# Kernel optimization log

Measured on AMD Instinct MI355X. Metric: run time of the kernel, lower is better.

The kernel has to match this reference:

```python
import jax, jax.numpy as jnp
import numpy as np

S, T, B, E, H, V = 64, 64, 64, 256, 256, 32000
PAD = 0


def _lstm_layer(X, Wih, Whh, b, h0, c0):
    # X: (time, B, in), torch gate order i,f,g,o
    def step(carry, x_t):
        h, c = carry
        z = x_t @ Wih.T + h @ Whh.T + b
        i, f, g, o = jnp.split(z, 4, axis=-1)
        c = jax.nn.sigmoid(f) * c + jax.nn.sigmoid(i) * jnp.tanh(g)
        h = jax.nn.sigmoid(o) * jnp.tanh(c)
        return (h, c), h
    (hT, cT), outs = jax.lax.scan(step, (h0, c0), X)
    return outs, hT, cT


def setup_inputs() -> dict:
    key = jax.random.key(0)
    ks = jax.random.split(key, 20)
    p = lambda k, shape: (jax.random.normal(k, shape, jnp.float32) * 0.05)
    inp = {
        "source_padded": jax.random.randint(ks[0], (S, B), 0, V, jnp.int32),
        "target_padded": jax.random.randint(ks[1], (T, B), 0, V, jnp.int32),
        "src_emb": p(ks[2], (V, E)),
        "tgt_emb": p(ks[3], (V, E)),
        "enc_Wih_f": p(ks[4], (4 * H, E)),
        "enc_Whh_f": p(ks[5], (4 * H, H)),
        "enc_b_f": p(ks[6], (4 * H,)),
        "enc_Wih_b": p(ks[7], (4 * H, E)),
        "enc_Whh_b": p(ks[8], (4 * H, H)),
        "enc_b_b": p(ks[9], (4 * H,)),
        "dec_Wih": p(ks[10], (4 * H, E + H)),
        "dec_Whh": p(ks[11], (4 * H, H)),
        "dec_b": p(ks[12], (4 * H,)),
        "Wh": p(ks[13], (H, 2 * H)),
        "Wc": p(ks[14], (H, 2 * H)),
        "Watt": p(ks[15], (H, 2 * H)),
        "Wcomb": p(ks[16], (H, 3 * H)),
        "Wvocab": p(ks[17], (V, H)),
    }
    return inp


def reference(source_padded, target_padded, src_emb, tgt_emb,
              enc_Wih_f, enc_Whh_f, enc_b_f, enc_Wih_b, enc_Whh_b, enc_b_b,
              dec_Wih, dec_Whh, dec_b, Wh, Wc, Watt, Wcomb, Wvocab):
    X = src_emb[source_padded]                      # (S,B,E)
    h0 = jnp.zeros((B, H), X.dtype)
    c0 = jnp.zeros((B, H), X.dtype)
    # bidirectional encoder (all sequences full length -> pack is identity)
    fwd_out, hf, cf = _lstm_layer(X, enc_Wih_f, enc_Whh_f, enc_b_f, h0, c0)
    bwd_out, hb, cb = _lstm_layer(X[::-1], enc_Wih_b, enc_Whh_b, enc_b_b, h0, c0)
    bwd_out = bwd_out[::-1]
    enc_hiddens = jnp.concatenate([fwd_out, bwd_out], -1).transpose(1, 0, 2)  # (B,S,2H)
    dec_h = jnp.concatenate([hf, hb], -1) @ Wh.T     # h_projection
    dec_c = jnp.concatenate([cf, cb], -1) @ Wc.T     # c_projection
    enc_proj = enc_hiddens @ Watt.T                  # (B,S,H)

    Y = tgt_emb[target_padded[:-1]]                  # (T-1,B,E)

    def dstep(carry, Y_t):
        h, c, o_prev = carry
        x = jnp.concatenate([Y_t, o_prev], -1)       # (B,E+H)
        z = x @ dec_Wih.T + h @ dec_Whh.T + dec_b
        i, f, g, o = jnp.split(z, 4, axis=-1)
        c = jax.nn.sigmoid(f) * c + jax.nn.sigmoid(i) * jnp.tanh(g)
        h = jax.nn.sigmoid(o) * jnp.tanh(c)
        e_t = jnp.einsum('bsh,bh->bs', enc_proj, h)  # attention scores
        alpha = jax.nn.softmax(e_t, axis=-1)         # no pads -> mask is no-op
        a_t = jnp.einsum('bs,bsd->bd', alpha, enc_hiddens)  # context (B,2H)
        O_t = jnp.tanh(jnp.concatenate([a_t, h], -1) @ Wcomb.T)  # dropout=eval
        return (h, c, O_t), O_t

    _, outs = jax.lax.scan(dstep, (dec_h, dec_c, jnp.zeros((B, H), X.dtype)), Y)
    P = jax.nn.log_softmax(outs @ Wvocab.T, axis=-1)          # (T-1,B,V)
    gold = jnp.take_along_axis(P, target_padded[1:][..., None], axis=-1)[..., 0]
    tmask = (target_padded[1:] != PAD).astype(P.dtype)
    return (gold * tmask).sum(axis=0)                          # (B,)
```

## Files before the change

### kernel.cpp

```cpp
#include <hip/hip_runtime.h>
#include <hip/hip_bf16.h>

static constexpr int S = 64, T = 64, B = 64, E = 256, H = 256, V = 32000;
static constexpr int H4 = 4 * H;
static constexpr int NCHUNK = 500;
static constexpr int NROW = (T - 1) * B;
static constexpr int LDP = 264;

typedef short bf16x8 __attribute__((ext_vector_type(8)));
typedef float f32x4 __attribute__((ext_vector_type(4)));
typedef unsigned long long ull;

__device__ __forceinline__ float sigf(float x) { return 1.0f / (1.0f + __expf(-x)); }
__device__ __forceinline__ float tanhfast(float x) { return 1.0f - 2.0f / (__expf(2.0f * x) + 1.0f); }
__device__ __forceinline__ float bflo(uint w) { return __uint_as_float(w << 16); }
__device__ __forceinline__ float bfhi(uint w) { return __uint_as_float(w & 0xffff0000u); }
__device__ __forceinline__ ushort f2bu(float x) {
  return __bfloat16_as_ushort(__float2bfloat16(x));
}

__device__ __forceinline__ void st_u32(uint* p, uint v) {
  __hip_atomic_store(p, v, __ATOMIC_RELAXED, __HIP_MEMORY_SCOPE_AGENT);
}
__device__ __forceinline__ uint ld_u32(const uint* p) {
  return __hip_atomic_load(p, __ATOMIC_RELAXED, __HIP_MEMORY_SCOPE_AGENT);
}

__global__ __launch_bounds__(256) void k_cvt_bf16(const float* __restrict__ src,
                                                  __hip_bfloat16* __restrict__ dst, int n) {
  int i = blockIdx.x * 256 + threadIdx.x;
  if (i < n) dst[i] = __float2bfloat16(src[i]);
}

__global__ __launch_bounds__(256) void k_cvt_slice(const float* __restrict__ src,
                                                   __hip_bfloat16* __restrict__ dst) {
  int n = blockIdx.x, tid = threadIdx.x;
  dst[n * 256 + tid] = __float2bfloat16(src[n * 512 + tid]);
}

__global__ __launch_bounds__(256) void k_gather(const int* __restrict__ idx,
                                                const float* __restrict__ emb,
                                                __hip_bfloat16* __restrict__ dst) {
  int r = blockIdx.x, tid = threadIdx.x;
  dst[r * 256 + tid] = __float2bfloat16(emb[idx[r] * E + tid]);
}

__global__ __launch_bounds__(256) void k_pack4(const float* __restrict__ src,
                                               uint2* __restrict__ dst,
                                               int total, int jshift, int ld, int off) {
  int idx = blockIdx.x * 256 + threadIdx.x;
  if (idx >= total) return;
  int J = 1 << jshift;
  int i = idx >> jshift, j = idx & (J - 1);
  const float* s = src + (size_t)j * ld + off + 4 * i;
  float4 v = *(const float4*)s;
  uint2 o;
  o.x = (uint)f2bu(v.x) | ((uint)f2bu(v.y) << 16);
  o.y = (uint)f2bu(v.z) | ((uint)f2bu(v.w) << 16);
  dst[(size_t)i * J + j] = o;
}

#define MFMA_TILE_BODY(Abase, Wbase, rb, cb)                                     \
  const int tid = threadIdx.x;                                                   \
  const int lane = tid & 63, wid = tid >> 6;                                     \
  const int wr = wid >> 1, wc = wid & 1;                                         \
  const int l15 = lane & 15, l4 = lane >> 4;                                     \
  for (int it = 0; it < 8; it++) {                                               \
    int c = it * 256 + tid;                                                      \
    int row = c >> 5, off = (c & 31) * 8;                                        \
    *(uint4*)&Asl[row * LDP + off] =                                             \
        *(const uint4*)((Abase) + (size_t)((rb) + row) * 256 + off);             \
    *(uint4*)&Bsl[row * LDP + off] =                                             \
        *(const uint4*)((Wbase) + (size_t)((cb) + row) * 256 + off);             \
  }                                                                              \
  __syncthreads();                                                               \
  f32x4 acc[2][2];                                                               \
  for (int m = 0; m < 2; m++)                                                    \
    for (int n = 0; n < 2; n++) acc[m][n] = (f32x4){0.f, 0.f, 0.f, 0.f};         \
  for (int kk = 0; kk < 8; kk++) {                                               \
    int ko = kk * 32 + l4 * 8;                                                   \
    bf16x8 a0 = *(const bf16x8*)&Asl[(wr * 32 + l15) * LDP + ko];                \
    bf16x8 a1 = *(const bf16x8*)&Asl[(wr * 32 + 16 + l15) * LDP + ko];           \
    bf16x8 b0 = *(const bf16x8*)&Bsl[(wc * 32 + l15) * LDP + ko];                \
    bf16x8 b1 = *(const bf16x8*)&Bsl[(wc * 32 + 16 + l15) * LDP + ko];           \
    acc[0][0] = __builtin_amdgcn_mfma_f32_16x16x32_bf16(a0, b0, acc[0][0], 0, 0, 0); \
    acc[0][1] = __builtin_amdgcn_mfma_f32_16x16x32_bf16(a0, b1, acc[0][1], 0, 0, 0); \
    acc[1][0] = __builtin_amdgcn_mfma_f32_16x16x32_bf16(a1, b0, acc[1][0], 0, 0, 0); \
    acc[1][1] = __builtin_amdgcn_mfma_f32_16x16x32_bf16(a1, b1, acc[1][1], 0, 0, 0); \
  }

__global__ __launch_bounds__(256) void k_gemm_bias(
    const __hip_bfloat16* __restrict__ A, const __hip_bfloat16* __restrict__ W,
    const float* __restrict__ bias, float* __restrict__ C, int ldc) {
  __shared__ __align__(16) ushort Asl[64 * LDP];
  __shared__ __align__(16) ushort Bsl[64 * LDP];
  const int cb = blockIdx.x * 64, rb = blockIdx.y * 64;
  MFMA_TILE_BODY((const ushort*)A, (const ushort*)W, rb, cb)
  #pragma unroll
  for (int m = 0; m < 2; m++)
    #pragma unroll
    for (int n = 0; n < 2; n++) {
      int col = cb + wc * 32 + n * 16 + l15;
      float bv = bias[col];
      #pragma unroll
      for (int r = 0; r < 4; r++) {
        int row = rb + wr * 32 + m * 16 + l4 * 4 + r;
        C[(size_t)row * ldc + col] = acc[m][n][r] + bv;
      }
    }
}

__global__ __launch_bounds__(256) void k_encproj_mfma(
    const __hip_bfloat16* __restrict__ fwd_bf, const __hip_bfloat16* __restrict__ bwd_bf,
    const __hip_bfloat16* __restrict__ Watt_bf, __hip_bfloat16* __restrict__ encproj_bf) {
  __shared__ __align__(16) ushort Asl[64 * LDP];
  __shared__ __align__(16) ushort Bsl[64 * LDP];
  const int cb = blockIdx.x * 64, rb = blockIdx.y * 64;
  const int tid = threadIdx.x;
  const int lane = tid & 63, wid = tid >> 6;
  const int wr = wid >> 1, wc = wid & 1;
  const int l15 = lane & 15, l4 = lane >> 4;
  f32x4 acc[2][2];
  #pragma unroll
  for (int m = 0; m < 2; m++)
    #pragma unroll
    for (int n = 0; n < 2; n++) acc[m][n] = (f32x4){0.f, 0.f, 0.f, 0.f};
  for (int kt = 0; kt < 2; kt++) {
    if (kt) __syncthreads();
    for (int it = 0; it < 8; it++) {
      int c = it * 256 + tid;
      int row = c >> 5, off = (c & 31) * 8;
      int r = rb + row, s = r >> 6, bb = r & 63;
      const ushort* arow = (kt == 0)
          ? (const ushort*)fwd_bf + (size_t)(s * 64 + bb) * 256
          : (const ushort*)bwd_bf + (size_t)(s * 64 + bb) * 256;
      *(uint4*)&Asl[row * LDP + off] = *(const uint4*)(arow + off);
      *(uint4*)&Bsl[row * LDP + off] =
          *(const uint4*)((const ushort*)Watt_bf + (size_t)(cb + row) * 512 + kt * 256 + off);
    }
    __syncthreads();
    for (int kk = 0; kk < 8; kk++) {
      int ko = kk * 32 + l4 * 8;
      bf16x8 a0 = *(const bf16x8*)&Asl[(wr * 32 + l15) * LDP + ko];
      bf16x8 a1 = *(const bf16x8*)&Asl[(wr * 32 + 16 + l15) * LDP + ko];
      bf16x8 b0 = *(const bf16x8*)&Bsl[(wc * 32 + l15) * LDP + ko];
      bf16x8 b1 = *(const bf16x8*)&Bsl[(wc * 32 + 16 + l15) * LDP + ko];
      acc[0][0] = __builtin_amdgcn_mfma_f32_16x16x32_bf16(a0, b0, acc[0][0], 0, 0, 0);
      acc[0][1] = __builtin_amdgcn_mfma_f32_16x16x32_bf16(a0, b1, acc[0][1], 0, 0, 0);
      acc[1][0] = __builtin_amdgcn_mfma_f32_16x16x32_bf16(a1, b0, acc[1][0], 0, 0, 0);
      acc[1][1] = __builtin_amdgcn_mfma_f32_16x16x32_bf16(a1, b1, acc[1][1], 0, 0, 0);
    }
  }
  #pragma unroll
  for (int m = 0; m < 2; m++)
    #pragma unroll
    for (int n = 0; n < 2; n++) {
      int col = cb + wc * 32 + n * 16 + l15;
      #pragma unroll
      for (int r = 0; r < 4; r++) {
        int row = rb + wr * 32 + m * 16 + l4 * 4 + r;
        int s = row >> 6, bb = row & 63;
        ((ushort*)encproj_bf)[(size_t)(bb * 64 + s) * 256 + col] = f2bu(acc[m][n][r]);
      }
    }
}

__global__ __launch_bounds__(256) void k_vocab2(
    const __hip_bfloat16* __restrict__ outs_bf, const __hip_bfloat16* __restrict__ Wv,
    const int* __restrict__ tgt, float* __restrict__ part_max,
    float* __restrict__ part_sum, float* __restrict__ gold) {
  __shared__ __align__(16) ushort Asl[64 * LDP];
  __shared__ __align__(16) ushort Bsl[64 * LDP];
  __shared__ int goldcol[64];
  __shared__ float pm[64][2], ps[64][2];
  const int vb = blockIdx.x;
  const int tid = threadIdx.x;
  const int lane = tid & 63, wid = tid >> 6;
  const int wr = wid >> 1, wc = wid & 1;
  const int l15 = lane & 15, l4 = lane >> 4;
  for (int it = 0; it < 8; it++) {
    int c = it * 256 + tid;
    int row = c >> 5, off = (c & 31) * 8;
    *(uint4*)&Bsl[row * LDP + off] =
        *(const uint4*)((const ushort*)Wv + (size_t)(vb * 64 + row) * 256 + off);
  }
  for (int t = 0; t < T - 1; t++) {
    __syncthreads();
    for (int it = 0; it < 8; it++) {
      int c = it * 256 + tid;
      int row = c >> 5, off = (c & 31) * 8;
      *(uint4*)&Asl[row * LDP + off] =
          *(const uint4*)((const ushort*)outs_bf + (size_t)(t * 64 + row) * 256 + off);
    }
    if (tid < 64) goldcol[tid] = tgt[(t + 1) * B + tid];
    __syncthreads();
    f32x4 acc[2][2];
    #pragma unroll
    for (int m = 0; m < 2; m++)
      #pragma unroll
      for (int n = 0; n < 2; n++) acc[m][n] = (f32x4){0.f, 0.f, 0.f, 0.f};
    for (int kk = 0; kk < 8; kk++) {
      int ko = kk * 32 + l4 * 8;
      bf16x8 a0 = *(const bf16x8*)&Asl[(wr * 32 + l15) * LDP + ko];
      bf16x8 a1 = *(const bf16x8*)&Asl[(wr * 32 + 16 + l15) * LDP + ko];
      bf16x8 b0 = *(const bf16x8*)&Bsl[(wc * 32 + l15) * LDP + ko];
      bf16x8 b1 = *(const bf16x8*)&Bsl[(wc * 32 + 16 + l15) * LDP + ko];
      acc[0][0] = __builtin_amdgcn_mfma_f32_16x16x32_bf16(a0, b0, acc[0][0], 0, 0, 0);
      acc[0][1] = __builtin_amdgcn_mfma_f32_16x16x32_bf16(a0, b1, acc[0][1], 0, 0, 0);
      acc[1][0] = __builtin_amdgcn_mfma_f32_16x16x32_bf16(a1, b0, acc[1][0], 0, 0, 0);
      acc[1][1] = __builtin_amdgcn_mfma_f32_16x16x32_bf16(a1, b1, acc[1][1], 0, 0, 0);
    }
    #pragma unroll
    for (int m = 0; m < 2; m++) {
      #pragma unroll
      for (int r = 0; r < 4; r++) {
        int row_local = wr * 32 + m * 16 + l4 * 4 + r;
        int gc = goldcol[row_local];
        #pragma unroll
        for (int n = 0; n < 2; n++) {
          int col = vb * 64 + wc * 32 + n * 16 + l15;
          if (col == gc) gold[t * 64 + row_local] = acc[m][n][r];
        }
        float v = fmaxf(acc[m][0][r], acc[m][1][r]);
        #pragma unroll
        for (int o = 1; o < 16; o <<= 1) v = fmaxf(v, __shfl_xor(v, o));
        float e = __expf(acc[m][0][r] - v) + __expf(acc[m][1][r] - v);
        #pragma unroll
        for (int o = 1; o < 16; o <<= 1) e += __shfl_xor(e, o);
        if (l15 == 0) { pm[row_local][wc] = v; ps[row_local][wc] = e; }
      }
    }
    __syncthreads();
    if (tid < 64) {
      float m0 = pm[tid][0], m1 = pm[tid][1];
      float M = fmaxf(m0, m1);
      float Ss = ps[tid][0] * __expf(m0 - M) + ps[tid][1] * __expf(m1 - M);
      part_max[(size_t)vb * NROW + t * 64 + tid] = M;
      part_sum[(size_t)vb * NROW + t * 64 + tid] = Ss;
    }
  }
}

__global__ __launch_bounds__(256) void k_enc4(
    const float* __restrict__ XwF, const float* __restrict__ XwB,
    const float* __restrict__ WhhF, const float* __restrict__ WhhB,
    uint* __restrict__ Xenc_u32,
    __hip_bfloat16* __restrict__ fwd_bf, __hip_bfloat16* __restrict__ bwd_bf,
    float* __restrict__ Cfin, uint* __restrict__ eflags) {
  __shared__ __align__(16) ushort Wl[128 * 264];
  __shared__ __align__(16) ushort Xa[16 * 264];
  __shared__ float zz[4][8][33];
  __shared__ float hsb[8][32];
  const int id = blockIdx.x;
  const int g = id & 7, kb = id >> 3;
  const int dir = kb >> 3, s = kb & 7;
  const int tid = threadIdx.x;
  const float* Whh = dir ? WhhB : WhhF;
  const float* Xw = dir ? XwB : XwF;
  uint* fl = eflags + (size_t)(g * 2 + dir) * 8 * 32;
  for (int i = tid; i < 128 * 256; i += 256) {
    int c = i >> 8, k2 = i & 255;
    int gate = c >> 5, jj = c & 31;
    Wl[c * 264 + k2] = f2bu(Whh[(size_t)(gate * 256 + s * 32 + jj) * 256 + k2]);
  }
  for (int i = tid; i < 16 * 264; i += 256) Xa[i] = 0;
  const int lane = tid & 63, w = tid >> 6;
  const int l15 = lane & 15, l4 = lane >> 4;
  const int tb = tid >> 5, tjj = tid & 31;
  float c_reg = 0.f;
  __syncthreads();
  for (int st = 0; st < 64; st++) {
    const int ts = dir ? 63 - st : st;
    const int par = st & 1;
    const uint* Xr = Xenc_u32 + (size_t)(par * 2 + dir) * 8192;
    uint* Xo = Xenc_u32 + (size_t)((par ^ 1) * 2 + dir) * 8192;
    for (int i = tid; i < 8 * 128; i += 256) {
      int row = i >> 7, colu = i & 127;
      uint v = ld_u32(Xr + (size_t)(8 * g + row) * 128 + colu);
      *(uint*)&Xa[row * 264 + colu * 2] = v;
    }
    __syncthreads();
    f32x4 a0v = (f32x4){0.f, 0.f, 0.f, 0.f}, a1v = (f32x4){0.f, 0.f, 0.f, 0.f};
    for (int kk = 0; kk < 8; kk++) {
      bf16x8 af = *(const bf16x8*)&Xa[l15 * 264 + kk * 32 + l4 * 8];
      bf16x8 b0 = *(const bf16x8*)&Wl[((2 * w) * 16 + l15) * 264 + kk * 32 + l4 * 8];
      bf16x8 b1 = *(const bf16x8*)&Wl[((2 * w + 1) * 16 + l15) * 264 + kk * 32 + l4 * 8];
      a0v = __builtin_amdgcn_mfma_f32_16x16x32_bf16(af, b0, a0v, 0, 0, 0);
      a1v = __builtin_amdgcn_mfma_f32_16x16x32_bf16(af, b1, a1v, 0, 0, 0);
    }
    if (l4 < 2) {
      #pragma unroll
      for (int r = 0; r < 4; r++) {
        int b = l4 * 4 + r;
        zz[w][b][l15] = a0v[r];
        zz[w][b][16 + l15] = a1v[r];
      }
    }
    __syncthreads();
    {
      int gb = 8 * g + tb, j = 32 * s + tjj;
      const float* xw = Xw + (size_t)(ts * 64 + gb) * 1024;
      float zi = zz[0][tb][tjj] + xw[j];
      float zf = zz[1][tb][tjj] + xw[256 + j];
      float zg = zz[2][tb][tjj] + xw[512 + j];
      float zo = zz[3][tb][tjj] + xw[768 + j];
      float c = sigf(zf) * c_reg + sigf(zi) * tanhfast(zg);
      c_reg = c;
      float h = sigf(zo) * tanhfast(c);
      hsb[tb][tjj] = h;
      ushort hb = f2bu(h);
      if (dir == 0) ((ushort*)fwd_bf)[(size_t)(st * 64 + gb) * 256 + j] = hb;
      else          ((ushort*)bwd_bf)[(size_t)((63 - st) * 64 + gb) * 256 + j] = hb;
    }
    __syncthreads();
    if (tid < 128) {
      int tb2 = tid >> 4, p = tid & 15;
      uint v = (uint)f2bu(hsb[tb2][2 * p]) | ((uint)f2bu(hsb[tb2][2 * p + 1]) << 16);
      st_u32(Xo + (size_t)(8 * g + tb2) * 128 + 16 * s + p, v);
    }
    __syncthreads();
    if (tid == 0) st_u32(&fl[s * 32], (uint)(st + 1));
    if (tid < 8)
      while (ld_u32(&fl[tid * 32]) < (uint)(st + 1)) __builtin_amdgcn_s_sleep(2);
    asm volatile("" ::: "memory");
    __syncthreads();
  }
  Cfin[(size_t)(dir * 64 + 8 * g + tb) * 256 + 32 * s + tjj] = c_reg;
}

__global__ __launch_bounds__(256) void k_dec_init3(
    const __hip_bfloat16* __restrict__ Xenc, const float* __restrict__ Cfin,
    const float* __restrict__ Wh, const float* __restrict__ Wc,
    uint* __restrict__ Xd_u32, float* __restrict__ decc0) {
  int b = blockIdx.x, tid = threadIdx.x;
  __shared__ __align__(16) float ch[512], cc[512];
  __shared__ float hh[256];
  ch[tid]       = __bfloat162float(Xenc[(size_t)(0 * 64 + b) * 256 + tid]);
  ch[256 + tid] = __bfloat162float(Xenc[(size_t)(1 * 64 + b) * 256 + tid]);
  cc[tid]       = Cfin[(size_t)(0 * 64 + b) * 256 + tid];
  cc[256 + tid] = Cfin[(size_t)(1 * 64 + b) * 256 + tid];
  __syncthreads();
  const float* wh = Wh + tid * 512;
  const float* wc = Wc + tid * 512;
  float ah = 0, ac = 0;
  for (int k = 0; k < 512; k += 4) {
    float4 hv = *(const float4*)&ch[k];
    float4 cv = *(const float4*)&cc[k];
    float4 w1 = *(const float4*)&wh[k];
    float4 w2 = *(const float4*)&wc[k];
    ah += hv.x * w1.x + hv.y * w1.y + hv.z * w1.z + hv.w * w1.w;
    ac += cv.x * w2.x + cv.y * w2.y + cv.z * w2.z + cv.w * w2.w;
  }
  decc0[b * 256 + tid] = ac;
  hh[tid] = ah;
  __syncthreads();
  if (tid < 128) {
    uint v = (uint)f2bu(hh[2 * tid]) | ((uint)f2bu(hh[2 * tid + 1]) << 16);
    Xd_u32[(size_t)b * 256 + tid] = v;
    Xd_u32[(size_t)b * 256 + 128 + tid] = 0u;
  }
}

__global__ __launch_bounds__(512) void k_dec6(
    const float* __restrict__ YW, const float* __restrict__ dWih,
    const float* __restrict__ dWhh, const uint2* __restrict__ Wcq,
    const __hip_bfloat16* __restrict__ encproj_bf,
    const __hip_bfloat16* __restrict__ fwd_bf, const __hip_bfloat16* __restrict__ bwd_bf,
    const float* __restrict__ decc0, uint* __restrict__ Xd_u32,
    __hip_bfloat16* __restrict__ outs_bf,
    uint* __restrict__ zflags, uint* __restrict__ aflags) {
  __shared__ __align__(16) char smem[155648];
  const int id = blockIdx.x;
  const int g = id & 7, kb = id >> 3;
  const int tid = threadIdx.x;
  uint* zfl = zflags + (size_t)g * 8 * 32;
  uint* afl = aflags + (size_t)g * 16 * 32;

  if (kb < 8) {
    const int s = kb;
    ushort* Wl = (ushort*)smem;
    ushort* Xa = (ushort*)(smem + 133120);
    float* zslds = (float*)(smem + 149760);
    float* hsb = (float*)(smem + 153856);
    for (int i = tid; i < 128 * 512; i += 512) {
      int c = i >> 9, k2 = i & 511;
      int gate = c >> 5, jj = c & 31;
      int gr = gate * 256 + 32 * s + jj;
      float v = (k2 < 256) ? dWhh[(size_t)gr * 256 + k2]
                           : dWih[(size_t)gr * 512 + 256 + (k2 - 256)];
      Wl[c * 520 + k2] = f2bu(v);
    }
    for (int i = tid; i < 16 * 520; i += 512) Xa[i] = 0;
    const int lane = tid & 63, w = tid >> 6;
    const int l15 = lane & 15, l4 = lane >> 4;
    float c_reg = 0.f;
    if (tid < 256) {
      int b = tid >> 5, jj = tid & 31;
      c_reg = decc0[(size_t)(8 * g + b) * 256 + 32 * s + jj];
    }
    __syncthreads();
    for (int i = tid; i < 8 * 128; i += 512) {
      int row = i >> 7, p = i & 127;
      uint v = ld_u32(Xd_u32 + (size_t)(8 * g + row) * 256 + p);
      *(uint*)&Xa[row * 520 + 2 * p] = v;
    }
    __syncthreads();
    f32x4 accv = (f32x4){0.f, 0.f, 0.f, 0.f};
    for (int kk = 0; kk < 8; kk++) {
      bf16x8 af = *(const bf16x8*)&Xa[l15 * 520 + kk * 32 + l4 * 8];
      bf16x8 bf = *(const bf16x8*)&Wl[(w * 16 + l15) * 520 + kk * 32 + l4 * 8];
      accv = __builtin_amdgcn_mfma_f32_16x16x32_bf16(af, bf, accv, 0, 0, 0);
    }
    for (int t = 0; t < 63; t++) {
      const int par = t & 1;
      if (t > 0) {
        if (tid < 16)
          while (ld_u32(&afl[tid * 32]) < (uint)t) __builtin_amdgcn_s_sleep(1);
        asm volatile("" ::: "memory");
        __syncthreads();
      }
      for (int i = tid; i < 8 * 128; i += 512) {
        int row = i >> 7, p = i & 127;
        uint v = ld_u32(Xd_u32 + (size_t)par * 16384 + (size_t)(8 * g + row) * 256 + 128 + p);
        *(uint*)&Xa[row * 520 + 256 + 2 * p] = v;
      }
      __syncthreads();
      for (int kk = 8; kk < 16; kk++) {
        bf16x8 af = *(const bf16x8*)&Xa[l15 * 520 + kk * 32 + l4 * 8];
        bf16x8 bf = *(const bf16x8*)&Wl[(w * 16 + l15) * 520 + kk * 32 + l4 * 8];
        accv = __builtin_amdgcn_mfma_f32_16x16x32_bf16(af, bf, accv, 0, 0, 0);
      }
      if (l4 < 2) {
        #pragma unroll
        for (int r = 0; r < 4; r++) {
          int b = l4 * 4 + r;
          zslds[b * 128 + w * 16 + l15] = accv[r];
        }
      }
      __syncthreads();
      if (tid < 256) {
        int b = tid >> 5, jj = tid & 31;
        int gb = 8 * g + b;
        const float* yw = YW + (size_t)(t * 64 + gb) * 1024 + 32 * s + jj;
        float zi = zslds[b * 128 + jj] + yw[0];
        float zf = zslds[b * 128 + 32 + jj] + yw[256];
        float zg = zslds[b * 128 + 64 + jj] + yw[512];
        float zo = zslds[b * 128 + 96 + jj] + yw[768];
        float c = sigf(zf) * c_reg + sigf(zi) * tanhfast(zg);
        c_reg = c;
        hsb[b * 32 + jj] = sigf(zo) * tanhfast(c);
      }
      __syncthreads();
      if (tid < 128) {
        int b = tid >> 4, p = tid & 15;
        uint v = (uint)f2bu(hsb[b * 32 + 2 * p]) | ((uint)f2bu(hsb[b * 32 + 2 * p + 1]) << 16);
        st_u32(Xd_u32 + (size_t)(par ^ 1) * 16384 + (size_t)(8 * g + b) * 256 + 16 * s + p, v);
      }
      __syncthreads();
      if (tid == 0) st_u32(&zfl[s * 32], (uint)(t + 1));
      if (t < 62) {
        if (tid < 8)
          while (ld_u32(&zfl[tid * 32]) < (uint)(t + 1)) __builtin_amdgcn_s_sleep(1);
        asm volatile("" ::: "memory");
        __syncthreads();
        for (int i = tid; i < 8 * 128; i += 512) {
          int row = i >> 7, p = i & 127;
          uint v = ld_u32(Xd_u32 + (size_t)(par ^ 1) * 16384 + (size_t)(8 * g + row) * 256 + p);
          *(uint*)&Xa[row * 520 + 2 * p] = v;
        }
        __syncthreads();
        accv = (f32x4){0.f, 0.f, 0.f, 0.f};
        for (int kk = 0; kk < 8; kk++) {
          bf16x8 af = *(const bf16x8*)&Xa[l15 * 520 + kk * 32 + l4 * 8];
          bf16x8 bf = *(const bf16x8*)&Wl[(w * 16 + l15) * 520 + kk * 32 + l4 * 8];
          accv = __builtin_amdgcn_mfma_f32_16x16x32_bf16(af, bf, accv, 0, 0, 0);
        }
      }
    }
  } else {
    const int lb = (kb - 8) >> 1, jh = (kb - 8) & 1;
    const int b = 8 * g + lb;
    ushort* ep = (ushort*)smem;
    ushort* eh = (ushort*)(smem + 33792);
    float* hn = (float*)(smem + 100352);
    float* xcomb = (float*)(smem + 101376);
    float* e_l = (float*)(smem + 104448);
    float* alpha_l = (float*)(smem + 104704);
    float* op_l = (float*)(smem + 104960);
    float* Ost = (float*)(smem + 107008);
    for (int i = tid; i < 64 * 256; i += 512) {
      int s2 = i >> 8, k2 = i & 255;
      ep[s2 * 264 + k2] = ((const ushort*)encproj_bf)[(size_t)(b * 64 + s2) * 256 + k2];
    }
    for (int i = tid; i < 64 * 512; i += 512) {
      int s2 = i >> 9, d = i & 511;
      ushort v = (d < 256) ? ((const ushort*)fwd_bf)[(size_t)(s2 * 64 + b) * 256 + d]
                           : ((const ushort*)bwd_bf)[(size_t)(s2 * 64 + b) * 256 + d - 256];
      eh[s2 * 520 + d] = v;
    }
    __syncthreads();
    for (int t = 0; t < 63; t++) {
      if (tid < 8)
        while (ld_u32(&zfl[tid * 32]) < (uint)(t + 1)) __builtin_amdgcn_s_sleep(1);
      asm volatile("" ::: "memory");
      __syncthreads();
      if (tid < 128) {
        uint v = ld_u32(Xd_u32 + (size_t)((t & 1) ^ 1) * 16384 + (size_t)b * 256 + tid);
        hn[2 * tid] = bflo(v);
        hn[2 * tid + 1] = bfhi(v);
      }
      __syncthreads();
      {
        int s2 = tid >> 3, q8 = tid & 7;
        const ushort* pr = ep + s2 * 264 + q8 * 32;
        const float* hq = hn + q8 * 32;
        float a = 0.f;
        #pragma unroll 8
        for (int kk = 0; kk < 32; kk += 2) {
          uint wv = *(const uint*)(pr + kk);
          a += bflo(wv) * hq[kk] + bfhi(wv) * hq[kk + 1];
        }
        a += __shfl_xor(a, 1);
        a += __shfl_xor(a, 2);
        a += __shfl_xor(a, 4);
        if (q8 == 0) e_l[s2] = a;
      }
      __syncthreads();
      if (tid < 64) {
        float e = e_l[tid];
        float mx = e;
        #pragma unroll
        for (int o = 32; o > 0; o >>= 1) mx = fmaxf(mx, __shfl_xor(mx, o));
        float p = __expf(e - mx);
        float ss = p;
        #pragma unroll
        for (int o = 32; o > 0; o >>= 1) ss += __shfl_xor(ss, o);
        alpha_l[tid] = p / ss;
      }
      __syncthreads();
      {
        float a = 0.f;
        const ushort* col = eh + tid;
        #pragma unroll 8
        for (int s2 = 0; s2 < 64; s2++)
          a += alpha_l[s2] * __uint_as_float(((uint)col[s2 * 520]) << 16);
        xcomb[tid] = a;
        if (tid < 256) xcomb[512 + tid] = hn[tid];
      }
      __syncthreads();
      {
        int jl = tid & 127, kq = tid >> 7;
        int j = jh * 128 + jl;
        const uint2* wp = Wcq + (size_t)(kq * 48) * 256 + j;
        const float4* x4 = (const float4*)xcomb + kq * 48;
        float a = 0.f;
        #pragma unroll 6
        for (int ii = 0; ii < 48; ii++) {
          uint2 wv = wp[(size_t)ii * 256];
          float4 xv = x4[ii];
          a += bflo(wv.x) * xv.x + bfhi(wv.x) * xv.y + bflo(wv.y) * xv.z + bfhi(wv.y) * xv.w;
        }
        op_l[kq * 128 + jl] = a;
      }
      __syncthreads();
      if (tid < 128) {
        float sum = op_l[tid] + op_l[128 + tid] + op_l[256 + tid] + op_l[384 + tid];
        float O = tanhfast(sum);
        Ost[tid] = O;
        ((ushort*)outs_bf)[(size_t)(t * 64 + b) * 256 + jh * 128 + tid] = f2bu(O);
      }
      __syncthreads();
      if (tid < 64) {
        uint v = (uint)f2bu(Ost[2 * tid]) | ((uint)f2bu(Ost[2 * tid + 1]) << 16);
        st_u32(Xd_u32 + (size_t)((t & 1) ^ 1) * 16384 + (size_t)b * 256 + 128 + jh * 64 + tid, v);
      }
      __syncthreads();
      if (tid == 0) st_u32(&afl[(lb * 2 + jh) * 32], (uint)(t + 1));
    }
  }
}

__global__ __launch_bounds__(256) void k_final(
    const float* __restrict__ part_max, const float* __restrict__ part_sum,
    const float* __restrict__ gold, const int* __restrict__ tgt,
    float* __restrict__ out) {
  int b = blockIdx.x, tid = threadIdx.x;
  int tq = tid >> 2, q = tid & 3;
  __shared__ float lm[64][4], ls[64][4];
  __shared__ float red[64];
  if (tq < T - 1) {
    int n = tq * B + b;
    float m = -__builtin_inff(), s = 0;
    for (int i = q; i < NCHUNK; i += 4) {
      float pmv = part_max[(size_t)i * NROW + n];
      float psv = part_sum[(size_t)i * NROW + n];
      float M2 = fmaxf(m, pmv);
      s = s * __expf(m - M2) + psv * __expf(pmv - M2);
      m = M2;
    }
    lm[tq][q] = m;
    ls[tq][q] = s;
  }
  __syncthreads();
  if (tid < T - 1) {
    float M = fmaxf(fmaxf(lm[tid][0], lm[tid][1]), fmaxf(lm[tid][2], lm[tid][3]));
    float Ss = ls[tid][0] * __expf(lm[tid][0] - M) + ls[tid][1] * __expf(lm[tid][1] - M) +
               ls[tid][2] * __expf(lm[tid][2] - M) + ls[tid][3] * __expf(lm[tid][3] - M);
    float lse = M + logf(Ss);
    int g = tgt[(tid + 1) * B + b];
    red[tid] = (g != 0) ? (gold[tid * B + b] - lse) : 0.f;
  }
  if (tid == T - 1) red[T - 1] = 0.f;
  __syncthreads();
  if (tid == 0) {
    float s = 0;
    for (int i = 0; i < T - 1; i++) s += red[i];
    out[b] = s;
  }
}

extern "C" void kernel_launch(void* const* d_in, const int* in_sizes, int n_in,
                              void* d_out, int out_size, void* d_ws, size_t ws_size,
                              hipStream_t stream) {
  (void)in_sizes; (void)n_in; (void)out_size; (void)ws_size;
  const int*   src   = (const int*)  d_in[0];
  const int*   tgt   = (const int*)  d_in[1];
  const float* semb  = (const float*)d_in[2];
  const float* temb  = (const float*)d_in[3];
  const float* WihF  = (const float*)d_in[4];
  const float* WhhF  = (const float*)d_in[5];
  const float* bF    = (const float*)d_in[6];
  const float* WihB  = (const float*)d_in[7];
  const float* WhhB  = (const float*)d_in[8];
  const float* bB    = (const float*)d_in[9];
  const float* dWih  = (const float*)d_in[10];
  const float* dWhh  = (const float*)d_in[11];
  const float* db    = (const float*)d_in[12];
  const float* Wh    = (const float*)d_in[13];
  const float* Wc    = (const float*)d_in[14];
  const float* Watt  = (const float*)d_in[15];
  const float* Wcomb = (const float*)d_in[16];
  const float* Wv    = (const float*)d_in[17];
  float* out = (float*)d_out;

  char* wp = (char*)d_ws;
  auto alloc = [&](size_t bytes) -> char* {
    char* p = wp;
    wp += (bytes + 255) & ~(size_t)255;
    return p;
  };
  float* XwF  = (float*)alloc((size_t)S * B * H4 * 4);
  float* XwB  = (float*)alloc((size_t)S * B * H4 * 4);
  float* YW   = (float*)alloc((size_t)(T - 1) * B * H4 * 4);
  __hip_bfloat16* fwd_bf     = (__hip_bfloat16*)alloc((size_t)S * B * H * 2);
  __hip_bfloat16* bwd_bf     = (__hip_bfloat16*)alloc((size_t)S * B * H * 2);
  __hip_bfloat16* encproj_bf = (__hip_bfloat16*)alloc((size_t)B * S * H * 2);
  __hip_bfloat16* Ag         = (__hip_bfloat16*)alloc((size_t)S * B * E * 2);
  __hip_bfloat16* Yg         = (__hip_bfloat16*)alloc((size_t)(T - 1) * B * E * 2);
  __hip_bfloat16* WihF_bf    = (__hip_bfloat16*)alloc((size_t)H4 * E * 2);
  __hip_bfloat16* WihB_bf    = (__hip_bfloat16*)alloc((size_t)H4 * E * 2);
  __hip_bfloat16* dWih_bf    = (__hip_bfloat16*)alloc((size_t)H4 * E * 2);
  __hip_bfloat16* Wv_bf      = (__hip_bfloat16*)alloc((size_t)V * H * 2);
  __hip_bfloat16* Watt_bf    = (__hip_bfloat16*)alloc((size_t)H * 512 * 2);
  __hip_bfloat16* outs_bf    = (__hip_bfloat16*)alloc((size_t)NROW * H * 2);
  uint2* Wcq = (uint2*)alloc((size_t)192 * 256 * 8);
  float* part_max = (float*)alloc((size_t)NCHUNK * NROW * 4);
  float* part_sum = (float*)alloc((size_t)NCHUNK * NROW * 4);
  float* gold     = (float*)alloc((size_t)NROW * 4);
  float* Cfin  = (float*)alloc((size_t)2 * B * H * 4);
  float* decc0 = (float*)alloc((size_t)B * H * 4);
  __hip_bfloat16* Xenc = (__hip_bfloat16*)alloc((size_t)2 * 2 * B * H * 2);
  uint* Xdec = (uint*)alloc((size_t)2 * B * 256 * 4);
  char* stateBase = wp;
  uint* eflags = (uint*)alloc(16 * 8 * 32 * 4);
  uint* zflags = (uint*)alloc(8 * 8 * 32 * 4);
  uint* aflags = (uint*)alloc(8 * 16 * 32 * 4);
  size_t stateBytes = (size_t)(wp - stateBase);
  hipMemsetAsync(stateBase, 0, stateBytes, stream);
  hipMemsetAsync(Xenc, 0, (size_t)2 * 2 * B * H * 2, stream);

  hipLaunchKernelGGL(k_cvt_bf16, dim3((H4 * E + 255) / 256), dim3(256), 0, stream,
                     WihF, WihF_bf, H4 * E);
  hipLaunchKernelGGL(k_cvt_bf16, dim3((H4 * E + 255) / 256), dim3(256), 0, stream,
                     WihB, WihB_bf, H4 * E);
  hipLaunchKernelGGL(k_cvt_slice, dim3(H4), dim3(256), 0, stream, dWih, dWih_bf);
  hipLaunchKernelGGL(k_cvt_bf16, dim3((V * H + 255) / 256), dim3(256), 0, stream,
                     Wv, Wv_bf, V * H);
  hipLaunchKernelGGL(k_cvt_bf16, dim3((H * 512 + 255) / 256), dim3(256), 0, stream,
                     Watt, Watt_bf, H * 512);
  hipLaunchKernelGGL(k_gather, dim3(S * B), dim3(256), 0, stream, src, semb, Ag);
  hipLaunchKernelGGL(k_gather, dim3((T - 1) * B), dim3(256), 0, stream, tgt, temb, Yg);
  hipLaunchKernelGGL(k_pack4, dim3(192 * 256 / 256), dim3(256), 0, stream,
                     Wcomb, Wcq, 192 * 256, 8, 768, 0);

  hipLaunchKernelGGL(k_gemm_bias, dim3(H4 / 64, S * B / 64), dim3(256), 0, stream,
                     Ag, WihF_bf, bF, XwF, H4);
  hipLaunchKernelGGL(k_gemm_bias, dim3(H4 / 64, S * B / 64), dim3(256), 0, stream,
                     Ag, WihB_bf, bB, XwB, H4);
  hipLaunchKernelGGL(k_gemm_bias, dim3(H4 / 64, (T - 1) * B / 64), dim3(256), 0, stream,
                     Yg, dWih_bf, db, YW, H4);

  hipLaunchKernelGGL(k_enc4, dim3(128), dim3(256), 0, stream,
                     XwF, XwB, WhhF, WhhB, (uint*)Xenc, fwd_bf, bwd_bf, Cfin, eflags);
  hipLaunchKernelGGL(k_dec_init3, dim3(B), dim3(256), 0, stream,
                     Xenc, Cfin, Wh, Wc, Xdec, decc0);
  hipLaunchKernelGGL(k_encproj_mfma, dim3(4, 64), dim3(256), 0, stream,
                     fwd_bf, bwd_bf, Watt_bf, encproj_bf);

  hipLaunchKernelGGL(k_dec6, dim3(192), dim3(512), 0, stream,
                     YW, dWih, dWhh, Wcq, encproj_bf, fwd_bf, bwd_bf,
                     decc0, Xdec, outs_bf, zflags, aflags);

  hipLaunchKernelGGL(k_vocab2, dim3(NCHUNK), dim3(256), 0, stream,
                     outs_bf, Wv_bf, tgt, part_max, part_sum, gold);
  hipLaunchKernelGGL(k_final, dim3(B), dim3(256), 0, stream,
                     part_max, part_sum, gold, tgt, out);
}
```

Baseline: 1.209 ms.

## Fuse embedding gather and weight conversion into GEMMs and encoder kernel

The embedding gather and the fp32-to-bf16 weight casts now happen inside the input-projection GEMM's shared-memory load, so the separate conversion and gather kernels and their intermediate buffers go away. The Wv, Watt and Wcomb conversions run on 64 extra blocks added to the encoder recurrence kernel, overlapping with the serial LSTM work. The decoder input projection is launched after the encoder. In the encoder and decoder steps, hidden-state bf16 packing now pairs values with a lane shuffle and stores them directly, removing an LDS staging buffer and one barrier per step. The extra blocks compete with the encoder recurrence for resources, and the GEMMs now re-read fp32 weights once per tile.

```diff
diff --git a/kernel.cpp b/kernel.cpp
--- a/kernel.cpp
+++ b/kernel.cpp
@@ -18,6 +18,9 @@
 __device__ __forceinline__ ushort f2bu(float x) {
   return __bfloat16_as_ushort(__float2bfloat16(x));
 }
+__device__ __forceinline__ uint packbf(float a, float b) {
+  return (uint)f2bu(a) | ((uint)f2bu(b) << 16);
+}
 
 __device__ __forceinline__ void st_u32(uint* p, uint v) {
   __hip_atomic_store(p, v, __ATOMIC_RELAXED, __HIP_MEMORY_SCOPE_AGENT);
@@ -26,76 +29,52 @@
   return __hip_atomic_load(p, __ATOMIC_RELAXED, __HIP_MEMORY_SCOPE_AGENT);
 }
 
-__global__ __launch_bounds__(256) void k_cvt_bf16(const float* __restrict__ src,
-                                                  __hip_bfloat16* __restrict__ dst, int n) {
-  int i = blockIdx.x * 256 + threadIdx.x;
-  if (i < n) dst[i] = __float2bfloat16(src[i]);
-}
-
-__global__ __launch_bounds__(256) void k_cvt_slice(const float* __restrict__ src,
-                                                   __hip_bfloat16* __restrict__ dst) {
-  int n = blockIdx.x, tid = threadIdx.x;
-  dst[n * 256 + tid] = __float2bfloat16(src[n * 512 + tid]);
-}
-
-__global__ __launch_bounds__(256) void k_gather(const int* __restrict__ idx,
-                                                const float* __restrict__ emb,
-                                                __hip_bfloat16* __restrict__ dst) {
-  int r = blockIdx.x, tid = threadIdx.x;
-  dst[r * 256 + tid] = __float2bfloat16(emb[idx[r] * E + tid]);
-}
-
-__global__ __launch_bounds__(256) void k_pack4(const float* __restrict__ src,
-                                               uint2* __restrict__ dst,
-                                               int total, int jshift, int ld, int off) {
-  int idx = blockIdx.x * 256 + threadIdx.x;
-  if (idx >= total) return;
-  int J = 1 << jshift;
-  int i = idx >> jshift, j = idx & (J - 1);
-  const float* s = src + (size_t)j * ld + off + 4 * i;
-  float4 v = *(const float4*)s;
-  uint2 o;
-  o.x = (uint)f2bu(v.x) | ((uint)f2bu(v.y) << 16);
-  o.y = (uint)f2bu(v.z) | ((uint)f2bu(v.w) << 16);
-  dst[(size_t)i * J + j] = o;
-}
-
-#define MFMA_TILE_BODY(Abase, Wbase, rb, cb)                                     \
-  const int tid = threadIdx.x;                                                   \
-  const int lane = tid & 63, wid = tid >> 6;                                     \
-  const int wr = wid >> 1, wc = wid & 1;                                         \
-  const int l15 = lane & 15, l4 = lane >> 4;                                     \
-  for (int it = 0; it < 8; it++) {                                               \
-    int c = it * 256 + tid;                                                      \
-    int row = c >> 5, off = (c & 31) * 8;                                        \
-    *(uint4*)&Asl[row * LDP + off] =                                             \
-        *(const uint4*)((Abase) + (size_t)((rb) + row) * 256 + off);             \
-    *(uint4*)&Bsl[row * LDP + off] =                                             \
-        *(const uint4*)((Wbase) + (size_t)((cb) + row) * 256 + off);             \
-  }                                                                              \
-  __syncthreads();                                                               \
-  f32x4 acc[2][2];                                                               \
-  for (int m = 0; m < 2; m++)                                                    \
-    for (int n = 0; n < 2; n++) acc[m][n] = (f32x4){0.f, 0.f, 0.f, 0.f};         \
-  for (int kk = 0; kk < 8; kk++) {                                               \
-    int ko = kk * 32 + l4 * 8;                                                   \
-    bf16x8 a0 = *(const bf16x8*)&Asl[(wr * 32 + l15) * LDP + ko];                \
-    bf16x8 a1 = *(const bf16x8*)&Asl[(wr * 32 + 16 + l15) * LDP + ko];           \
-    bf16x8 b0 = *(const bf16x8*)&Bsl[(wc * 32 + l15) * LDP + ko];                \
-    bf16x8 b1 = *(const bf16x8*)&Bsl[(wc * 32 + 16 + l15) * LDP + ko];           \
-    acc[0][0] = __builtin_amdgcn_mfma_f32_16x16x32_bf16(a0, b0, acc[0][0], 0, 0, 0); \
-    acc[0][1] = __builtin_amdgcn_mfma_f32_16x16x32_bf16(a0, b1, acc[0][1], 0, 0, 0); \
-    acc[1][0] = __builtin_amdgcn_mfma_f32_16x16x32_bf16(a1, b0, acc[1][0], 0, 0, 0); \
-    acc[1][1] = __builtin_amdgcn_mfma_f32_16x16x32_bf16(a1, b1, acc[1][1], 0, 0, 0); \
-  }
-
-__global__ __launch_bounds__(256) void k_gemm_bias(
-    const __hip_bfloat16* __restrict__ A, const __hip_bfloat16* __restrict__ W,
-    const float* __restrict__ bias, float* __restrict__ C, int ldc) {
+__global__ __launch_bounds__(256) void k_gemm_gather(
+    const int* __restrict__ idx, const float* __restrict__ emb,
+    const float* __restrict__ W, int wld, const float* __restrict__ bias,
+    float* __restrict__ C, int ldc) {
   __shared__ __align__(16) ushort Asl[64 * LDP];
   __shared__ __align__(16) ushort Bsl[64 * LDP];
   const int cb = blockIdx.x * 64, rb = blockIdx.y * 64;
-  MFMA_TILE_BODY((const ushort*)A, (const ushort*)W, rb, cb)
+  const int tid = threadIdx.x;
+  const int lane = tid & 63, wid = tid >> 6;
+  const int wr = wid >> 1, wc = wid & 1;
+  const int l15 = lane & 15, l4 = lane >> 4;
+  for (int it = 0; it < 8; it++) {
+    int c = it * 256 + tid;
+    int row = c >> 5, off = (c & 31) * 8;
+    const float* asrc = emb + (size_t)idx[rb + row] * 256 + off;
+    float4 a0 = *(const float4*)asrc;
+    float4 a1 = *(const float4*)(asrc + 4);
+    uint4 av;
+    av.x = packbf(a0.x, a0.y); av.y = packbf(a0.z, a0.w);
+    av.z = packbf(a1.x, a1.y); av.w = packbf(a1.z, a1.w);
+    *(uint4*)&Asl[row * LDP + off] = av;
+    const float* bsrc = W + (size_t)(cb + row) * wld + off;
+    float4 b0 = *(const float4*)bsrc;
+    float4 b1 = *(const float4*)(bsrc + 4);
+    uint4 bv;
+    bv.x = packbf(b0.x, b0.y); bv.y = packbf(b0.z, b0.w);
+    bv.z = packbf(b1.x, b1.y); bv.w = packbf(b1.z, b1.w);
+    *(uint4*)&Bsl[row * LDP + off] = bv;
+  }
+  __syncthreads();
+  f32x4 acc[2][2];
+  #pragma unroll
+  for (int m = 0; m < 2; m++)
+    #pragma unroll
+    for (int n = 0; n < 2; n++) acc[m][n] = (f32x4){0.f, 0.f, 0.f, 0.f};
+  for (int kk = 0; kk < 8; kk++) {
+    int ko = kk * 32 + l4 * 8;
+    bf16x8 a0 = *(const bf16x8*)&Asl[(wr * 32 + l15) * LDP + ko];
+    bf16x8 a1 = *(const bf16x8*)&Asl[(wr * 32 + 16 + l15) * LDP + ko];
+    bf16x8 b0 = *(const bf16x8*)&Bsl[(wc * 32 + l15) * LDP + ko];
+    bf16x8 b1 = *(const bf16x8*)&Bsl[(wc * 32 + 16 + l15) * LDP + ko];
+    acc[0][0] = __builtin_amdgcn_mfma_f32_16x16x32_bf16(a0, b0, acc[0][0], 0, 0, 0);
+    acc[0][1] = __builtin_amdgcn_mfma_f32_16x16x32_bf16(a0, b1, acc[0][1], 0, 0, 0);
+    acc[1][0] = __builtin_amdgcn_mfma_f32_16x16x32_bf16(a1, b0, acc[1][0], 0, 0, 0);
+    acc[1][1] = __builtin_amdgcn_mfma_f32_16x16x32_bf16(a1, b1, acc[1][1], 0, 0, 0);
+  }
   #pragma unroll
   for (int m = 0; m < 2; m++)
     #pragma unroll
@@ -166,7 +145,7 @@
 }
 
 __global__ __launch_bounds__(256) void k_vocab2(
-    const __hip_bfloat16* __restrict__ outs_bf, const __hip_bfloat16* __restrict__ Wv,
+    const uint* __restrict__ outs_u, const __hip_bfloat16* __restrict__ Wv,
     const int* __restrict__ tgt, float* __restrict__ part_max,
     float* __restrict__ part_sum, float* __restrict__ gold) {
   __shared__ __align__(16) ushort Asl[64 * LDP];
@@ -186,11 +165,10 @@
   }
   for (int t = 0; t < T - 1; t++) {
     __syncthreads();
-    for (int it = 0; it < 8; it++) {
-      int c = it * 256 + tid;
-      int row = c >> 5, off = (c & 31) * 8;
-      *(uint4*)&Asl[row * LDP + off] =
-          *(const uint4*)((const ushort*)outs_bf + (size_t)(t * 64 + row) * 256 + off);
+    for (int i = tid; i < 64 * 128; i += 256) {
+      int row = i >> 7, colu = i & 127;
+      uint v = outs_u[(size_t)(t * 64 + row) * 128 + colu];
+      *(uint*)&Asl[row * LDP + colu * 2] = v;
     }
     if (tid < 64) goldcol[tid] = tgt[(t + 1) * B + tid];
     __syncthreads();
@@ -241,20 +219,43 @@
   }
 }
 
-__global__ __launch_bounds__(256) void k_enc4(
+__global__ __launch_bounds__(256) void k_enc4w(
     const float* __restrict__ XwF, const float* __restrict__ XwB,
     const float* __restrict__ WhhF, const float* __restrict__ WhhB,
     uint* __restrict__ Xenc_u32,
     __hip_bfloat16* __restrict__ fwd_bf, __hip_bfloat16* __restrict__ bwd_bf,
-    float* __restrict__ Cfin, uint* __restrict__ eflags) {
+    float* __restrict__ Cfin, uint* __restrict__ eflags,
+    const float* __restrict__ Wv, __hip_bfloat16* __restrict__ Wv_bf,
+    const float* __restrict__ Watt, __hip_bfloat16* __restrict__ Watt_bf,
+    const float* __restrict__ Wcomb, uint2* __restrict__ Wcq) {
   __shared__ __align__(16) ushort Wl[128 * 264];
   __shared__ __align__(16) ushort Xa[16 * 264];
   __shared__ float zz[4][8][33];
-  __shared__ float hsb[8][32];
   const int id = blockIdx.x;
+  const int tid = threadIdx.x;
+  if (id >= 128) {
+    const int wtid = (id - 128) * 256 + tid;
+    const int wn = 64 * 256;
+    for (int i = wtid; i < (V * H) / 4; i += wn) {
+      float4 v = ((const float4*)Wv)[i];
+      uint2 o; o.x = packbf(v.x, v.y); o.y = packbf(v.z, v.w);
+      ((uint2*)Wv_bf)[i] = o;
+    }
+    for (int i = wtid; i < (H * 512) / 4; i += wn) {
+      float4 v = ((const float4*)Watt)[i];
+      uint2 o; o.x = packbf(v.x, v.y); o.y = packbf(v.z, v.w);
+      ((uint2*)Watt_bf)[i] = o;
+    }
+    for (int i2 = wtid; i2 < 192 * 256; i2 += wn) {
+      int i = i2 >> 8, j = i2 & 255;
+      float4 v = *(const float4*)(Wcomb + (size_t)j * 768 + 4 * i);
+      uint2 o; o.x = packbf(v.x, v.y); o.y = packbf(v.z, v.w);
+      Wcq[(size_t)i * 256 + j] = o;
+    }
+    return;
+  }
   const int g = id & 7, kb = id >> 3;
   const int dir = kb >> 3, s = kb & 7;
-  const int tid = threadIdx.x;
   const float* Whh = dir ? WhhB : WhhF;
   const float* Xw = dir ? XwB : XwF;
   uint* fl = eflags + (size_t)(g * 2 + dir) * 8 * 32;
@@ -307,16 +308,12 @@
       float c = sigf(zf) * c_reg + sigf(zi) * tanhfast(zg);
       c_reg = c;
       float h = sigf(zo) * tanhfast(c);
-      hsb[tb][tjj] = h;
       ushort hb = f2bu(h);
       if (dir == 0) ((ushort*)fwd_bf)[(size_t)(st * 64 + gb) * 256 + j] = hb;
       else          ((ushort*)bwd_bf)[(size_t)((63 - st) * 64 + gb) * 256 + j] = hb;
-    }
-    __syncthreads();
-    if (tid < 128) {
-      int tb2 = tid >> 4, p = tid & 15;
-      uint v = (uint)f2bu(hsb[tb2][2 * p]) | ((uint)f2bu(hsb[tb2][2 * p + 1]) << 16);
-      st_u32(Xo + (size_t)(8 * g + tb2) * 128 + 16 * s + p, v);
+      float hp = __shfl_xor(h, 1);
+      if ((tjj & 1) == 0)
+        st_u32(Xo + (size_t)gb * 128 + 16 * s + (tjj >> 1), packbf(h, hp));
     }
     __syncthreads();
     if (tid == 0) st_u32(&fl[s * 32], (uint)(st + 1));
@@ -355,8 +352,7 @@
   hh[tid] = ah;
   __syncthreads();
   if (tid < 128) {
-    uint v = (uint)f2bu(hh[2 * tid]) | ((uint)f2bu(hh[2 * tid + 1]) << 16);
-    Xd_u32[(size_t)b * 256 + tid] = v;
+    Xd_u32[(size_t)b * 256 + tid] = packbf(hh[2 * tid], hh[2 * tid + 1]);
     Xd_u32[(size_t)b * 256 + 128 + tid] = 0u;
   }
 }
@@ -367,9 +363,9 @@
     const __hip_bfloat16* __restrict__ encproj_bf,
     const __hip_bfloat16* __restrict__ fwd_bf, const __hip_bfloat16* __restrict__ bwd_bf,
     const float* __restrict__ decc0, uint* __restrict__ Xd_u32,
-    __hip_bfloat16* __restrict__ outs_bf,
+    uint* __restrict__ outs_u,
     uint* __restrict__ zflags, uint* __restrict__ aflags) {
-  __shared__ __align__(16) char smem[155648];
+  __shared__ __align__(16) char smem[154112];
   const int id = blockIdx.x;
   const int g = id & 7, kb = id >> 3;
   const int tid = threadIdx.x;
@@ -381,7 +377,6 @@
     ushort* Wl = (ushort*)smem;
     ushort* Xa = (ushort*)(smem + 133120);
     float* zslds = (float*)(smem + 149760);
-    float* hsb = (float*)(smem + 153856);
     for (int i = tid; i < 128 * 512; i += 512) {
       int c = i >> 9, k2 = i & 511;
       int gate = c >> 5, jj = c & 31;
@@ -448,13 +443,11 @@
         float zo = zslds[b * 128 + 96 + jj] + yw[768];
         float c = sigf(zf) * c_reg + sigf(zi) * tanhfast(zg);
         c_reg = c;
-        hsb[b * 32 + jj] = sigf(zo) * tanhfast(c);
-      }
-      __syncthreads();
-      if (tid < 128) {
-        int b = tid >> 4, p = tid & 15;
-        uint v = (uint)f2bu(hsb[b * 32 + 2 * p]) | ((uint)f2bu(hsb[b * 32 + 2 * p + 1]) << 16);
-        st_u32(Xd_u32 + (size_t)(par ^ 1) * 16384 + (size_t)(8 * g + b) * 256 + 16 * s + p, v);
+        float h = sigf(zo) * tanhfast(c);
+        float hp = __shfl_xor(h, 1);
+        if ((jj & 1) == 0)
+          st_u32(Xd_u32 + (size_t)(par ^ 1) * 16384 + (size_t)gb * 256 + 16 * s + (jj >> 1),
+                 packbf(h, hp));
       }
       __syncthreads();
       if (tid == 0) st_u32(&zfl[s * 32], (uint)(t + 1));
@@ -487,7 +480,6 @@
     float* e_l = (float*)(smem + 104448);
     float* alpha_l = (float*)(smem + 104704);
     float* op_l = (float*)(smem + 104960);
-    float* Ost = (float*)(smem + 107008);
     for (int i = tid; i < 64 * 256; i += 512) {
       int s2 = i >> 8, k2 = i & 255;
       ep[s2 * 264 + k2] = ((const ushort*)encproj_bf)[(size_t)(b * 64 + s2) * 256 + k2];
@@ -566,13 +558,12 @@
       if (tid < 128) {
         float sum = op_l[tid] + op_l[128 + tid] + op_l[256 + tid] + op_l[384 + tid];
         float O = tanhfast(sum);
-        Ost[tid] = O;
-        ((ushort*)outs_bf)[(size_t)(t * 64 + b) * 256 + jh * 128 + tid] = f2bu(O);
-      }
-      __syncthreads();
-      if (tid < 64) {
-        uint v = (uint)f2bu(Ost[2 * tid]) | ((uint)f2bu(Ost[2 * tid + 1]) << 16);
-        st_u32(Xd_u32 + (size_t)((t & 1) ^ 1) * 16384 + (size_t)b * 256 + 128 + jh * 64 + tid, v);
+        float Op = __shfl_xor(O, 1);
+        if ((tid & 1) == 0) {
+          uint v = packbf(O, Op);
+          st_u32(Xd_u32 + (size_t)((t & 1) ^ 1) * 16384 + (size_t)b * 256 + 128 + jh * 64 + (tid >> 1), v);
+          st_u32(outs_u + (size_t)(t * 64 + b) * 128 + jh * 64 + (tid >> 1), v);
+        }
       }
       __syncthreads();
       if (tid == 0) st_u32(&afl[(lb * 2 + jh) * 32], (uint)(t + 1));
@@ -655,14 +646,9 @@
   __hip_bfloat16* fwd_bf     = (__hip_bfloat16*)alloc((size_t)S * B * H * 2);
   __hip_bfloat16* bwd_bf     = (__hip_bfloat16*)alloc((size_t)S * B * H * 2);
   __hip_bfloat16* encproj_bf = (__hip_bfloat16*)alloc((size_t)B * S * H * 2);
-  __hip_bfloat16* Ag         = (__hip_bfloat16*)alloc((size_t)S * B * E * 2);
-  __hip_bfloat16* Yg         = (__hip_bfloat16*)alloc((size_t)(T - 1) * B * E * 2);
-  __hip_bfloat16* WihF_bf    = (__hip_bfloat16*)alloc((size_t)H4 * E * 2);
-  __hip_bfloat16* WihB_bf    = (__hip_bfloat16*)alloc((size_t)H4 * E * 2);
-  __hip_bfloat16* dWih_bf    = (__hip_bfloat16*)alloc((size_t)H4 * E * 2);
   __hip_bfloat16* Wv_bf      = (__hip_bfloat16*)alloc((size_t)V * H * 2);
   __hip_bfloat16* Watt_bf    = (__hip_bfloat16*)alloc((size_t)H * 512 * 2);
-  __hip_bfloat16* outs_bf    = (__hip_bfloat16*)alloc((size_t)NROW * H * 2);
+  uint* outs_u = (uint*)alloc((size_t)NROW * H * 2);
   uint2* Wcq = (uint2*)alloc((size_t)192 * 256 * 8);
   float* part_max = (float*)alloc((size_t)NCHUNK * NROW * 4);
   float* part_sum = (float*)alloc((size_t)NCHUNK * NROW * 4);
@@ -679,29 +665,17 @@
   hipMemsetAsync(stateBase, 0, stateBytes, stream);
   hipMemsetAsync(Xenc, 0, (size_t)2 * 2 * B * H * 2, stream);
 
-  hipLaunchKernelGGL(k_cvt_bf16, dim3((H4 * E + 255) / 256), dim3(256), 0, stream,
-                     WihF, WihF_bf, H4 * E);
-  hipLaunchKernelGGL(k_cvt_bf16, dim3((H4 * E + 255) / 256), dim3(256), 0, stream,
-                     WihB, WihB_bf, H4 * E);
-  hipLaunchKernelGGL(k_cvt_slice, dim3(H4), dim3(256), 0, stream, dWih, dWih_bf);
-  hipLaunchKernelGGL(k_cvt_bf16, dim3((V * H + 255) / 256), dim3(256), 0, stream,
-                     Wv, Wv_bf, V * H);
-  hipLaunchKernelGGL(k_cvt_bf16, dim3((H * 512 + 255) / 256), dim3(256), 0, stream,
-                     Watt, Watt_bf, H * 512);
-  hipLaunchKernelGGL(k_gather, dim3(S * B), dim3(256), 0, stream, src, semb, Ag);
-  hipLaunchKernelGGL(k_gather, dim3((T - 1) * B), dim3(256), 0, stream, tgt, temb, Yg);
-  hipLaunchKernelGGL(k_pack4, dim3(192 * 256 / 256), dim3(256), 0, stream,
-                     Wcomb, Wcq, 192 * 256, 8, 768, 0);
-
-  hipLaunchKernelGGL(k_gemm_bias, dim3(H4 / 64, S * B / 64), dim3(256), 0, stream,
-                     Ag, WihF_bf, bF, XwF, H4);
-  hipLaunchKernelGGL(k_gemm_bias, dim3(H4 / 64, S * B / 64), dim3(256), 0, stream,
-                     Ag, WihB_bf, bB, XwB, H4);
-  hipLaunchKernelGGL(k_gemm_bias, dim3(H4 / 64, (T - 1) * B / 64), dim3(256), 0, stream,
-                     Yg, dWih_bf, db, YW, H4);
-
-  hipLaunchKernelGGL(k_enc4, dim3(128), dim3(256), 0, stream,
-                     XwF, XwB, WhhF, WhhB, (uint*)Xenc, fwd_bf, bwd_bf, Cfin, eflags);
+  hipLaunchKernelGGL(k_gemm_gather, dim3(16, 64), dim3(256), 0, stream,
+                     src, semb, WihF, 256, bF, XwF, H4);
+  hipLaunchKernelGGL(k_gemm_gather, dim3(16, 64), dim3(256), 0, stream,
+                     src, semb, WihB, 256, bB, XwB, H4);
+
+  hipLaunchKernelGGL(k_enc4w, dim3(192), dim3(256), 0, stream,
+                     XwF, XwB, WhhF, WhhB, (uint*)Xenc, fwd_bf, bwd_bf, Cfin, eflags,
+                     Wv, Wv_bf, Watt, Watt_bf, Wcomb, Wcq);
+
+  hipLaunchKernelGGL(k_gemm_gather, dim3(16, 63), dim3(256), 0, stream,
+                     tgt, temb, dWih, 512, db, YW, H4);
   hipLaunchKernelGGL(k_dec_init3, dim3(B), dim3(256), 0, stream,
                      Xenc, Cfin, Wh, Wc, Xdec, decc0);
   hipLaunchKernelGGL(k_encproj_mfma, dim3(4, 64), dim3(256), 0, stream,
@@ -709,10 +683,10 @@
 
   hipLaunchKernelGGL(k_dec6, dim3(192), dim3(512), 0, stream,
                      YW, dWih, dWhh, Wcq, encproj_bf, fwd_bf, bwd_bf,
-                     decc0, Xdec, outs_bf, zflags, aflags);
+                     decc0, Xdec, outs_u, zflags, aflags);
 
   hipLaunchKernelGGL(k_vocab2, dim3(NCHUNK), dim3(256), 0, stream,
-                     outs_bf, Wv_bf, tgt, part_max, part_sum, gold);
+                     outs_u, Wv_bf, tgt, part_max, part_sum, gold);
   hipLaunchKernelGGL(k_final, dim3(B), dim3(256), 0, stream,
                      part_max, part_sum, gold, tgt, out);
 }
```

Result: no change. 1.230 ms (median of 2 runs) (+1.8%).
